# Optimization experiments

Hardware: AMD Instinct MI355X
Metric: run time of the kernel (lower is better)

The kernel has to match this reference:

```python
import jax, jax.numpy as jnp
import numpy as np

HID = 96
B = 64
PF = (HID + 1) ** 3  # 912673


def setup_inputs() -> dict:
    key = jax.random.key(0)
    ks = jax.random.split(key, 6)
    s1 = 1.0 / np.sqrt(PF)
    s2 = 1.0 / np.sqrt(HID)
    s3 = 1.0 / np.sqrt(HID // 2)
    return {
        "text_x": jax.random.normal(ks[0], (B, HID), jnp.float32),
        "audio_x": jax.random.normal(ks[1], (B, HID), jnp.float32),
        "video_x": jax.random.normal(ks[2], (B, HID), jnp.float32),
        "W1": jax.random.normal(ks[3], (HID, PF), jnp.float32) * s1,
        "b1": jnp.zeros((HID,), jnp.float32),
        "W2": jax.random.normal(ks[4], (HID // 2, HID), jnp.float32) * s2,
        "b2": jnp.zeros((HID // 2,), jnp.float32),
        "W3": jax.random.normal(ks[5], (3, HID // 2), jnp.float32) * s3,
        "b3": jnp.zeros((3,), jnp.float32),
    }


def reference(text_x, audio_x, video_x, W1, b1, W2, b2, W3, b3):
    bsz = text_x.shape[0]
    ones = jnp.ones((bsz, 1), text_x.dtype)
    t = jnp.concatenate([ones, text_x], axis=1)   # [B, H+1]
    a = jnp.concatenate([ones, audio_x], axis=1)  # [B, H+1]
    v = jnp.concatenate([ones, video_x], axis=1)  # [B, H+1]
    # outer product of the three modalities, flattened: [B, (H+1)^3]
    fusion = jnp.einsum("bi,bj,bk->bijk", t, a, v).reshape(bsz, -1)
    # post-fusion MLP (dropout is identity at inference)
    h = jax.nn.relu(fusion @ W1.T + b1)
    h = jax.nn.relu(h @ W2.T + b2)
    return h @ W3.T + b3
```

## Files before the change

### kernel.cpp

```cpp
#include <hip/hip_runtime.h>
#include <stdint.h>


#define HID    96
#define NP1    97
#define ROWLEN 9409
#define NBLK   9312
#define BATCH  64
#define RSTR   104

typedef short bf16x8 __attribute__((ext_vector_type(8)));
typedef float f32x4  __attribute__((ext_vector_type(4)));

__device__ __forceinline__ uint32_t pack2bf(float lo, float hi) {
    union { float f; uint32_t u; } a, b; a.f = lo; b.f = hi;
    uint32_t ra = (a.u + 0x7fffu + ((a.u >> 16) & 1u)) >> 16;
    uint32_t rb = (b.u + 0x7fffu + ((b.u >> 16) & 1u)) & 0xffff0000u;
    return ra | rb;
}

__global__ __launch_bounds__(256, 6)
void fusion_gemm(const float* __restrict__ W1,
                 const float* __restrict__ text_x,
                 const float* __restrict__ audio_x,
                 const float* __restrict__ video_x,
                 float* __restrict__ h1pre)
{
    __shared__ __align__(16) short Wbf[NP1 * RSTR];
    __shared__ float biasF[NP1];

    const int tid = threadIdx.x;
    const int blk = blockIdx.x;
    const int o = blk / 97;
    const int i = blk - o * 97;
    const float* Wt = W1 + (long)blk * ROWLEN;

    for (int j = tid; j < NP1; j += 256) biasF[j] = Wt[j * NP1];

    for (int w = tid; w < NP1 * 12; w += 256) {
        int j = w / 12;
        int s = w - j * 12;
        const float* p = Wt + j * NP1 + 1 + s * 8;
        uint4 q;
        q.x = pack2bf(p[0], p[1]);
        q.y = pack2bf(p[2], p[3]);
        q.z = pack2bf(p[4], p[5]);
        q.w = pack2bf(p[6], p[7]);
        *reinterpret_cast<uint4*>(&Wbf[j * RSTR + s * 8]) = q;
    }

    const int lane = tid & 63;
    const int wave = tid >> 6;
    const int quad = lane >> 4;
    const int col  = lane & 15;
    const int b    = wave * 16 + col;

    bf16x8 bfrag[3];
#pragma unroll
    for (int ks = 0; ks < 3; ++ks) {
        const float* vp = video_x + b * HID + ks * 32 + quad * 8;
        union { bf16x8 v; uint32_t d[4]; } u;
        u.d[0] = pack2bf(vp[0], vp[1]);
        u.d[1] = pack2bf(vp[2], vp[3]);
        u.d[2] = pack2bf(vp[4], vp[5]);
        u.d[3] = pack2bf(vp[6], vp[7]);
        bfrag[ks] = u.v;
    }

    __syncthreads();

    f32x4 acc[7];
#pragma unroll
    for (int mt = 0; mt < 7; ++mt) acc[mt] = (f32x4){0.f, 0.f, 0.f, 0.f};

#pragma unroll
    for (int ks = 0; ks < 3; ++ks) {
#pragma unroll
        for (int mt = 0; mt < 7; ++mt) {
            int j  = mt * 16 + col;
            int je = j > 96 ? 96 : j;
            bf16x8 af = *reinterpret_cast<const bf16x8*>(&Wbf[je * RSTR + ks * 32 + quad * 8]);
            acc[mt] = __builtin_amdgcn_mfma_f32_16x16x32_bf16(af, bfrag[ks], acc[mt], 0, 0, 0);
        }
    }

    float s = 0.f;
#pragma unroll
    for (int mt = 0; mt < 7; ++mt) {
#pragma unroll
        for (int r = 0; r < 4; ++r) {
            int j = mt * 16 + quad * 4 + r;
            if (j < 97) {
                float u  = acc[mt][r] + biasF[j];
                float aw = (j == 0) ? 1.f : audio_x[b * HID + (j - 1)];
                s += u * aw;
            }
        }
    }
    s += __shfl_xor(s, 16);
    s += __shfl_xor(s, 32);

    if (quad == 0) {
        float tw = (i == 0) ? 1.f : text_x[b * HID + (i - 1)];
        atomicAdd(&h1pre[o * BATCH + b], s * tw);
    }
}

__global__ __launch_bounds__(64)
void mlp_tail(const float* __restrict__ h1pre, const float* __restrict__ b1,
              const float* __restrict__ W2, const float* __restrict__ b2,
              const float* __restrict__ W3, const float* __restrict__ b3,
              float* __restrict__ out)
{
    __shared__ float h1s[96];
    __shared__ float h2s[48];
    const int b = blockIdx.x;
    const int t = threadIdx.x;
    for (int o = t; o < 96; o += 64) {
        float v = h1pre[o * BATCH + b] + b1[o];
        h1s[o] = v > 0.f ? v : 0.f;
    }
    __syncthreads();
    if (t < 48) {
        float acc = b2[t];
#pragma unroll 8
        for (int o = 0; o < 96; ++o) acc += W2[t * 96 + o] * h1s[o];
        h2s[t] = acc > 0.f ? acc : 0.f;
    }
    __syncthreads();
    if (t < 3) {
        float acc = b3[t];
#pragma unroll
        for (int c = 0; c < 48; ++c) acc += W3[t * 48 + c] * h2s[c];
        out[b * 3 + t] = acc;
    }
}

extern "C" void kernel_launch(void* const* d_in, const int* in_sizes, int n_in,
                              void* d_out, int out_size, void* d_ws, size_t ws_size,
                              hipStream_t stream)
{
    const float* text  = (const float*)d_in[0];
    const float* audio = (const float*)d_in[1];
    const float* video = (const float*)d_in[2];
    const float* W1    = (const float*)d_in[3];
    const float* b1    = (const float*)d_in[4];
    const float* W2    = (const float*)d_in[5];
    const float* b2    = (const float*)d_in[6];
    const float* W3    = (const float*)d_in[7];
    const float* b3    = (const float*)d_in[8];
    float* h1pre = (float*)d_ws;

    hipMemsetAsync(h1pre, 0, HID * BATCH * sizeof(float), stream);
    fusion_gemm<<<NBLK, 256, 0, stream>>>(W1, text, audio, video, h1pre);
    mlp_tail<<<BATCH, 64, 0, stream>>>(h1pre, b1, W2, b2, W3, b3, (float*)d_out);
}
```

Before: 539.9 us.

## Make fusion GEMM blocks persistent over i-slices with double-buffered LDS staging

Replaces the one-block-per-(o,i) grid of 9312 blocks with 768 blocks, each looping over about 12 i-slices of one output row. Each slice is staged into a double-buffered LDS tile while the previous one is consumed, and the audio weights are hoisted into registers. Per-slice results are summed in registers, so there is one atomic per block instead of one per slice. The cost is a grid of only 768 blocks, lower occupancy from twice the LDS and a launch bound of 3, and the prefetch being plain global loads issued before the MFMA work, which may limit how much they actually overlap.

```diff
diff --git a/kernel.cpp b/kernel.cpp
--- a/kernel.cpp
+++ b/kernel.cpp
@@ -5,7 +5,6 @@
 #define HID    96
 #define NP1    97
 #define ROWLEN 9409
-#define NBLK   9312
 #define BATCH  64
 #define RSTR   104
 
@@ -19,35 +18,21 @@
     return ra | rb;
 }
 
-__global__ __launch_bounds__(256, 6)
+__global__ __launch_bounds__(256, 3)
 void fusion_gemm(const float* __restrict__ W1,
                  const float* __restrict__ text_x,
                  const float* __restrict__ audio_x,
                  const float* __restrict__ video_x,
                  float* __restrict__ h1pre)
 {
-    __shared__ __align__(16) short Wbf[NP1 * RSTR];
-    __shared__ float biasF[NP1];
+    __shared__ __align__(16) short Wbf[2][NP1 * RSTR];
+    __shared__ float biasF[2][NP1];
 
     const int tid = threadIdx.x;
-    const int blk = blockIdx.x;
-    const int o = blk / 97;
-    const int i = blk - o * 97;
-    const float* Wt = W1 + (long)blk * ROWLEN;
-
-    for (int j = tid; j < NP1; j += 256) biasF[j] = Wt[j * NP1];
-
-    for (int w = tid; w < NP1 * 12; w += 256) {
-        int j = w / 12;
-        int s = w - j * 12;
-        const float* p = Wt + j * NP1 + 1 + s * 8;
-        uint4 q;
-        q.x = pack2bf(p[0], p[1]);
-        q.y = pack2bf(p[2], p[3]);
-        q.z = pack2bf(p[4], p[5]);
-        q.w = pack2bf(p[6], p[7]);
-        *reinterpret_cast<uint4*>(&Wbf[j * RSTR + s * 8]) = q;
-    }
+    const int o   = blockIdx.x >> 3;
+    const int c   = blockIdx.x & 7;
+    const int ilo = (c * 97) >> 3;
+    const int ihi = ((c + 1) * 97) >> 3;
 
     const int lane = tid & 63;
     const int wave = tid >> 6;
@@ -67,43 +52,74 @@
         bfrag[ks] = u.v;
     }
 
-    __syncthreads();
-
-    f32x4 acc[7];
+    float aval[28];
 #pragma unroll
-    for (int mt = 0; mt < 7; ++mt) acc[mt] = (f32x4){0.f, 0.f, 0.f, 0.f};
-
-#pragma unroll
-    for (int ks = 0; ks < 3; ++ks) {
-#pragma unroll
-        for (int mt = 0; mt < 7; ++mt) {
-            int j  = mt * 16 + col;
-            int je = j > 96 ? 96 : j;
-            bf16x8 af = *reinterpret_cast<const bf16x8*>(&Wbf[je * RSTR + ks * 32 + quad * 8]);
-            acc[mt] = __builtin_amdgcn_mfma_f32_16x16x32_bf16(af, bfrag[ks], acc[mt], 0, 0, 0);
-        }
-    }
-
-    float s = 0.f;
-#pragma unroll
-    for (int mt = 0; mt < 7; ++mt) {
+    for (int mt = 0; mt < 7; ++mt)
 #pragma unroll
         for (int r = 0; r < 4; ++r) {
             int j = mt * 16 + quad * 4 + r;
-            if (j < 97) {
-                float u  = acc[mt][r] + biasF[j];
-                float aw = (j == 0) ? 1.f : audio_x[b * HID + (j - 1)];
-                s += u * aw;
+            aval[mt * 4 + r] = (j == 0) ? 1.f
+                             : (j <= 96 ? audio_x[b * HID + (j - 1)] : 0.f);
+        }
+
+    auto stage = [&](int ii, int pbuf) {
+        const float* Wt = W1 + (long)(o * 97 + ii) * ROWLEN;
+        for (int j = tid; j < NP1; j += 256) biasF[pbuf][j] = Wt[j * NP1];
+        for (int w = tid; w < NP1 * 12; w += 256) {
+            int j = w / 12;
+            int s = w - j * 12;
+            const float* p = Wt + j * NP1 + 1 + s * 8;
+            uint4 q;
+            q.x = pack2bf(p[0], p[1]);
+            q.y = pack2bf(p[2], p[3]);
+            q.z = pack2bf(p[4], p[5]);
+            q.w = pack2bf(p[6], p[7]);
+            *reinterpret_cast<uint4*>(&Wbf[pbuf][j * RSTR + s * 8]) = q;
+        }
+    };
+
+    float sacc = 0.f;
+
+    stage(ilo, 0);
+    __syncthreads();
+
+    for (int ii = ilo; ii < ihi; ++ii) {
+        const int pb = (ii - ilo) & 1;
+        if (ii + 1 < ihi) stage(ii + 1, pb ^ 1);
+
+        f32x4 acc[7];
+#pragma unroll
+        for (int mt = 0; mt < 7; ++mt) acc[mt] = (f32x4){0.f, 0.f, 0.f, 0.f};
+#pragma unroll
+        for (int ks = 0; ks < 3; ++ks)
+#pragma unroll
+            for (int mt = 0; mt < 7; ++mt) {
+                int j  = mt * 16 + col;
+                int je = j > 96 ? 96 : j;
+                bf16x8 af = *reinterpret_cast<const bf16x8*>(
+                    &Wbf[pb][je * RSTR + ks * 32 + quad * 8]);
+                acc[mt] = __builtin_amdgcn_mfma_f32_16x16x32_bf16(af, bfrag[ks], acc[mt], 0, 0, 0);
             }
-        }
+
+        float s = 0.f;
+#pragma unroll
+        for (int mt = 0; mt < 7; ++mt)
+#pragma unroll
+            for (int r = 0; r < 4; ++r) {
+                int j  = mt * 16 + quad * 4 + r;
+                int je = j > 96 ? 96 : j;
+                s += (acc[mt][r] + biasF[pb][je]) * aval[mt * 4 + r];
+            }
+        s += __shfl_xor(s, 16);
+        s += __shfl_xor(s, 32);
+
+        float tw = (ii == 0) ? 1.f : text_x[b * HID + (ii - 1)];
+        sacc += s * tw;
+
+        __syncthreads();
     }
-    s += __shfl_xor(s, 16);
-    s += __shfl_xor(s, 32);
 
-    if (quad == 0) {
-        float tw = (i == 0) ? 1.f : text_x[b * HID + (i - 1)];
-        atomicAdd(&h1pre[o * BATCH + b], s * tw);
-    }
+    if (quad == 0) atomicAdd(&h1pre[o * BATCH + b], sacc);
 }
 
 __global__ __launch_bounds__(64)
@@ -152,6 +168,6 @@
     float* h1pre = (float*)d_ws;
 
     hipMemsetAsync(h1pre, 0, HID * BATCH * sizeof(float), stream);
-    fusion_gemm<<<NBLK, 256, 0, stream>>>(W1, text, audio, video, h1pre);
+    fusion_gemm<<<96 * 8, 256, 0, stream>>>(W1, text, audio, video, h1pre);
     mlp_tail<<<BATCH, 64, 0, stream>>>(h1pre, b1, W2, b2, W3, b3, (float*)d_out);
 }
```

Result: faster. 491.9 us (-8.9%).
